# Kernel tuning notes

Hardware: AMD Instinct MI355X
Metric: run time of the kernel (lower is better)

## Reference

```python
import jax, jax.numpy as jnp
import numpy as np

N, E, G = 20000, 320000, 64
IN_DIM, HID, HEADS, NCLS = 512, 256, 2, 10
EPS = 1e-5
SLOPE = 0.2


def setup_inputs() -> dict:
    key = jax.random.key(0)
    ks = jax.random.split(key, 24)
    s = 0.02
    inp = {
        "feat": jax.random.normal(ks[0], (N, IN_DIM), jnp.float32),
        "src": jax.random.randint(ks[1], (E,), 0, N, jnp.int32),
        "dst": jax.random.randint(ks[2], (E,), 0, N, jnp.int32),
        "graph_ids": jnp.sort(jax.random.randint(ks[3], (N,), 0, G, jnp.int32)),
        # GATv2Conv params (fc_src, fc_dst, attn)
        "W_src": jax.random.normal(ks[4], (IN_DIM, HEADS * HID), jnp.float32) * s,
        "b_src": jnp.zeros((HEADS * HID,), jnp.float32),
        "W_dst": jax.random.normal(ks[5], (IN_DIM, HEADS * HID), jnp.float32) * s,
        "b_dst": jnp.zeros((HEADS * HID,), jnp.float32),
        "attn": jax.random.normal(ks[6], (HEADS, HID), jnp.float32) * s,
        # skip_lin: input_dim -> 2*hidden
        "W_skip": jax.random.normal(ks[7], (IN_DIM, 2 * HID), jnp.float32) * s,
        "b_skip": jnp.zeros((2 * HID,), jnp.float32),
        # bn1 affine
        "gamma": jnp.ones((2 * HID,), jnp.float32),
        "beta": jnp.zeros((2 * HID,), jnp.float32),
        # dim_reducer
        "W_red": jax.random.normal(ks[8], (2 * HID, HID), jnp.float32) * s,
        "b_red": jnp.zeros((HID,), jnp.float32),
        # attention-pool gate Linear(hidden, 1)
        "w_gate": jax.random.normal(ks[9], (HID, 1), jnp.float32) * s,
        "b_gate": jnp.zeros((1,), jnp.float32),
        # classifier MLP
        "W1": jax.random.normal(ks[10], (HID, HID // 2), jnp.float32) * s,
        "b1": jnp.zeros((HID // 2,), jnp.float32),
        "W2": jax.random.normal(ks[11], (HID // 2, NCLS), jnp.float32) * s,
        "b2": jnp.zeros((NCLS,), jnp.float32),
    }
    return inp


def _gatv2(feat, src, dst, W_src, b_src, W_dst, b_dst, attn):
    # feat_src/feat_dst: [N, H, D]
    fs = (feat @ W_src + b_src).reshape(N, HEADS, HID)
    fd = (feat @ W_dst + b_dst).reshape(N, HEADS, HID)
    fs_e = fs[src]                               # [E, H, D]
    m = jax.nn.leaky_relu(fs_e + fd[dst], SLOPE)  # [E, H, D]
    e = jnp.einsum("ehd,hd->eh", m, attn)         # [E, H]
    # edge softmax grouped by destination node
    e_max = jax.ops.segment_max(e, dst, num_segments=N)          # [N, H]
    e_exp = jnp.exp(e - e_max[dst])                               # [E, H]
    denom = jax.ops.segment_sum(e_exp, dst, num_segments=N)      # [N, H]
    alpha = e_exp / denom[dst]                                    # [E, H]
    out = jax.ops.segment_sum(alpha[:, :, None] * fs_e, dst, num_segments=N)
    return out  # [N, H, D]; zero rows for zero in-degree nodes


def reference(feat, src, dst, graph_ids, W_src, b_src, W_dst, b_dst, attn,
              W_skip, b_skip, gamma, beta, W_red, b_red, w_gate, b_gate,
              W1, b1, W2, b2):
    h1 = jax.nn.elu(_gatv2(feat, src, dst, W_src, b_src, W_dst, b_dst, attn))
    h1 = h1.reshape(N, HEADS * HID)
    h1 = h1 + (feat @ W_skip + b_skip)
    # BatchNorm1d (training-mode batch statistics, biased variance)
    mu = jnp.mean(h1, axis=0)
    var = jnp.mean((h1 - mu) ** 2, axis=0)
    h1 = (h1 - mu) * jax.lax.rsqrt(var + EPS) * gamma + beta
    hr = h1 @ W_red + b_red                      # [N, HID]
    # GlobalAttentionPooling: segment softmax of gate scores over each graph
    gate = hr @ w_gate + b_gate                  # [N, 1]
    g_max = jax.ops.segment_max(gate, graph_ids, num_segments=G)
    g_exp = jnp.exp(gate - g_max[graph_ids])
    g_den = jax.ops.segment_sum(g_exp, graph_ids, num_segments=G)
    a = g_exp / g_den[graph_ids]                 # [N, 1]
    h_g = jax.ops.segment_sum(a * hr, graph_ids, num_segments=G)  # [G, HID]
    # classifier (dropout = identity at inference)
    return jax.nn.relu(h_g @ W1 + b1) @ W2 + b2  # [G, NCLS]
```

## Files before the change

### kernel.cpp

```cpp
#include <hip/hip_runtime.h>
#include <math.h>

#define N_NODES 20000
#define N_EDGES 320000
#define N_GRAPH 64
#define IN_DIM  512
#define HID     256
#define F2      512
#define EPS_BN  1e-5f
#define SLOPE   0.2f
#define SCAN_BLOCKS 79
#define N_RT    157
#define RT_PAD  20096

#define SF_BLOCKS   5024
#define SW_BLOCKS   1024
#define INIT_BLOCKS 79
#define PREP_BLOCKS (SF_BLOCKS + SW_BLOCKS + INIT_BLOCKS)
#define TRIPLE_BLOCKS 1920
#define HIST_BLOCKS   1250

typedef unsigned short u16;
typedef __attribute__((ext_vector_type(8))) short bf16x8;
typedef __attribute__((ext_vector_type(4))) float floatx4;

__device__ __forceinline__ u16 bf_hi(float x) {
    unsigned int u = __float_as_uint(x);
    return (u16)((u + 0x7fffu + ((u >> 16) & 1u)) >> 16);
}
__device__ __forceinline__ float bf_val(u16 h) {
    return __uint_as_float((unsigned int)h << 16);
}
__device__ __forceinline__ void unpack2(unsigned int u, float& lo, float& hi) {
    lo = __uint_as_float(u << 16);
    hi = __uint_as_float(u & 0xffff0000u);
}
__device__ __forceinline__ float lr(float x) { return fmaxf(x, SLOPE * x); }

__device__ __forceinline__ void gload16(const u16* g, u16* l) {
    __builtin_amdgcn_global_load_lds(
        (const __attribute__((address_space(1))) void*)g,
        (__attribute__((address_space(3))) void*)l, 16, 0, 0);
}

__global__ __launch_bounds__(256) void prep_kernel(
    const float* __restrict__ feat, u16* __restrict__ Fhi,
    const float* __restrict__ Ws, const float* __restrict__ Wd,
    const float* __restrict__ Wk, const float* __restrict__ Wr,
    u16* __restrict__ Whi, u16* __restrict__ Wlo,
    int* __restrict__ counts, int* __restrict__ cursor,
    float* __restrict__ stats, float* __restrict__ h_gnum,
    float* __restrict__ gden, float* __restrict__ gate) {
    __shared__ float t[32][33];
    int b = blockIdx.x;
    int tid = threadIdx.x;
    if (b < SF_BLOCKS) {
        int i = b * 256 + tid;
        size_t base = (size_t)i * 8;
        if (i >= N_NODES * IN_DIM / 8) {
            *(uint4*)(Fhi + base) = make_uint4(0, 0, 0, 0);
            return;
        }
        float4 x0 = *(const float4*)(feat + base);
        float4 x1 = *(const float4*)(feat + base + 4);
        float xs[8] = {x0.x, x0.y, x0.z, x0.w, x1.x, x1.y, x1.z, x1.w};
        union { u16 s[8]; uint4 v; } h;
#pragma unroll
        for (int j = 0; j < 8; j++) h.s[j] = bf_hi(xs[j]);
        *(uint4*)(Fhi + base) = h.v;
    } else if (b < SF_BLOCKS + SW_BLOCKS) {
        int bb = b - SF_BLOCKS;
        int kx = bb & 15, ny = (bb >> 4) & 15, w = bb >> 8;
        int ncols = (w == 3) ? 256 : 512;
        int n0 = ny * 32;
        if (n0 >= ncols) return;
        const float* W = (w == 0) ? Ws : ((w == 1) ? Wd : ((w == 2) ? Wk : Wr));
        size_t obase = (size_t)w * 512 * 512;
        int k0 = kx * 32;
        int tx = tid & 31, ty = tid >> 5;
#pragma unroll
        for (int i = 0; i < 4; i++)
            t[ty * 4 + i][tx] = W[(size_t)(k0 + ty * 4 + i) * ncols + n0 + tx];
        __syncthreads();
#pragma unroll
        for (int i = 0; i < 4; i++) {
            float x = t[tx][ty * 4 + i];
            u16 hh = bf_hi(x);
            size_t o = obase + (size_t)(n0 + ty * 4 + i) * 512 + k0 + tx;
            Whi[o] = hh;
            Wlo[o] = bf_hi(x - bf_val(hh));
        }
    } else {
        int i = (b - SF_BLOCKS - SW_BLOCKS) * 256 + tid;
        if (i < N_NODES) { counts[i] = 0; cursor[i] = 0; gate[i] = 0.f; }
        if (i < 1024) stats[i] = 0.f;
        if (i < N_GRAPH * HID) h_gnum[i] = 0.f;
        if (i < N_GRAPH) gden[i] = 0.f;
    }
}

__global__ __launch_bounds__(256) void gemm_mfma_triple(
    const u16* __restrict__ Fhi, const u16* __restrict__ Wthi,
    const float* __restrict__ b_src, const float* __restrict__ b_dst,
    const float* __restrict__ b_skip,
    u16* __restrict__ FS16, u16* __restrict__ FD16,
    u16* __restrict__ h1hi, u16* __restrict__ h1lo,
    const int* __restrict__ dst, int* __restrict__ counts) {
    __shared__ u16 S[2][2][8192];
    int b = blockIdx.x;
    if (b >= TRIPLE_BLOCKS) {
        int e = (b - TRIPLE_BLOCKS) * 256 + threadIdx.x;
        if (e < N_EDGES) atomicAdd(&counts[dst[e]], 1);
        return;
    }
    int xcd = b & 7, slot = b >> 3;
    int rt = (slot / 12) * 8 + xcd;
    if (rt >= N_RT) return;
    int cw = slot % 12;
    int w_idx = cw >> 2;
    int col0 = (cw & 3) * 128;
    int row0 = rt * 128;
    int tid = threadIdx.x;
    int lane = tid & 63, wave = tid >> 6;
    int wm = (wave & 1) * 64, wn = (wave >> 1) * 64;
    int quad = lane >> 4, l16 = lane & 15;

    int lrow = lane >> 3;
    int kswz = ((lane & 7) ^ lrow) << 3;
    const u16* aS = Fhi + (size_t)(row0 + wave * 32 + lrow) * 512 + kswz;
    const u16* bS = Wthi + (size_t)w_idx * 512 * 512 +
                    (size_t)(col0 + wave * 32 + lrow) * 512 + kswz;

#define STAGE(buf, kk)                                                        \
    do {                                                                      \
        gload16(aS + (size_t)(kk) * 64,         &S[buf][0][(wave * 4 + 0) * 512]); \
        gload16(bS + (size_t)(kk) * 64,         &S[buf][1][(wave * 4 + 0) * 512]); \
        gload16(aS + 4096 + (size_t)(kk) * 64,  &S[buf][0][(wave * 4 + 1) * 512]); \
        gload16(bS + 4096 + (size_t)(kk) * 64,  &S[buf][1][(wave * 4 + 1) * 512]); \
        gload16(aS + 8192 + (size_t)(kk) * 64,  &S[buf][0][(wave * 4 + 2) * 512]); \
        gload16(bS + 8192 + (size_t)(kk) * 64,  &S[buf][1][(wave * 4 + 2) * 512]); \
        gload16(aS + 12288 + (size_t)(kk) * 64, &S[buf][0][(wave * 4 + 3) * 512]); \
        gload16(bS + 12288 + (size_t)(kk) * 64, &S[buf][1][(wave * 4 + 3) * 512]); \
    } while (0)

    int kx8 = (l16 & 7) << 3;
    int oS0 = (quad * 8) ^ kx8;
    int offA = (wm + l16) * 64;
    int offB = (wn + l16) * 64;

    floatx4 acc[4][4];
#pragma unroll
    for (int i = 0; i < 4; i++)
#pragma unroll
        for (int j = 0; j < 4; j++) acc[i][j] = (floatx4){0.f, 0.f, 0.f, 0.f};

    STAGE(0, 0);
    __syncthreads();

#pragma unroll
    for (int kk = 0; kk < 8; kk++) {
        if (kk < 7) STAGE((kk + 1) & 1, kk + 1);
        const u16* A = &S[kk & 1][0][0];
        const u16* B = &S[kk & 1][1][0];
        bf16x8 bv[4][2];
#pragma unroll
        for (int nt = 0; nt < 4; nt++) {
            bv[nt][0] = *(const bf16x8*)&B[offB + nt * 1024 + oS0];
            bv[nt][1] = *(const bf16x8*)&B[offB + nt * 1024 + (oS0 ^ 32)];
        }
#pragma unroll
        for (int mt = 0; mt < 4; mt++) {
            bf16x8 a0 = *(const bf16x8*)&A[offA + mt * 1024 + oS0];
            bf16x8 a1 = *(const bf16x8*)&A[offA + mt * 1024 + (oS0 ^ 32)];
#pragma unroll
            for (int nt = 0; nt < 4; nt++) {
                acc[mt][nt] = __builtin_amdgcn_mfma_f32_16x16x32_bf16(
                    bv[nt][0], a0, acc[mt][nt], 0, 0, 0);
                acc[mt][nt] = __builtin_amdgcn_mfma_f32_16x16x32_bf16(
                    bv[nt][1], a1, acc[mt][nt], 0, 0, 0);
            }
        }
        __syncthreads();
    }
#undef STAGE

    const float* bias = (w_idx == 0) ? b_src : ((w_idx == 1) ? b_dst : b_skip);
    float4 b4[4];
#pragma unroll
    for (int wt = 0; wt < 4; wt++)
        b4[wt] = *(const float4*)(bias + col0 + wn + wt * 16 + quad * 4);
#pragma unroll
    for (int ft = 0; ft < 4; ft++) {
        int m = row0 + wm + ft * 16 + l16;
        if (m >= N_NODES) continue;
        size_t rb = (size_t)m * 512;
#pragma unroll
        for (int wt = 0; wt < 4; wt++) {
            int nb = col0 + wn + wt * 16 + quad * 4;
            float v0 = acc[ft][wt][0] + b4[wt].x;
            float v1 = acc[ft][wt][1] + b4[wt].y;
            float v2 = acc[ft][wt][2] + b4[wt].z;
            float v3 = acc[ft][wt][3] + b4[wt].w;
            u16 h0 = bf_hi(v0), h1_ = bf_hi(v1), h2 = bf_hi(v2), h3 = bf_hi(v3);
            uint2 wv;
            wv.x = (unsigned)h0 | ((unsigned)h1_ << 16);
            wv.y = (unsigned)h2 | ((unsigned)h3 << 16);
            if (w_idx == 0)      *(uint2*)(FS16 + rb + nb) = wv;
            else if (w_idx == 1) *(uint2*)(FD16 + rb + nb) = wv;
            else {
                *(uint2*)(h1hi + rb + nb) = wv;
                uint2 lv;
                lv.x = (unsigned)bf_hi(v0 - bf_val(h0)) | ((unsigned)bf_hi(v1 - bf_val(h1_)) << 16);
                lv.y = (unsigned)bf_hi(v2 - bf_val(h2)) | ((unsigned)bf_hi(v3 - bf_val(h3)) << 16);
                *(uint2*)(h1lo + rb + nb) = lv;
            }
        }
    }
}

__global__ __launch_bounds__(256) void scan_local_kernel(
    const int* __restrict__ counts, int* __restrict__ row_ptr, int* __restrict__ bsum) {
    __shared__ int buf[256];
    int b = blockIdx.x, tid = threadIdx.x;
    int i = b * 256 + tid;
    buf[tid] = (i < N_NODES) ? counts[i] : 0;
    __syncthreads();
    for (int off = 1; off < 256; off <<= 1) {
        int t = (tid >= off) ? buf[tid - off] : 0;
        __syncthreads();
        buf[tid] += t;
        __syncthreads();
    }
    if (i < N_NODES) row_ptr[i + 1] = buf[tid];
    if (tid == 255) bsum[b] = buf[255];
}

__global__ __launch_bounds__(256) void scan_fixup_kernel(
    const int* __restrict__ bsum, int* __restrict__ row_ptr) {
    __shared__ int red[256];
    int b = blockIdx.x, tid = threadIdx.x;
    red[tid] = (tid < b) ? bsum[tid] : 0;
    __syncthreads();
    for (int off = 128; off > 0; off >>= 1) {
        if (tid < off) red[tid] += red[tid + off];
        __syncthreads();
    }
    int offset = red[0];
    int i = b * 256 + tid;
    if (i < N_NODES) row_ptr[i + 1] += offset;
    if (b == 0 && tid == 0) row_ptr[0] = 0;
}

__global__ void scatter_kernel(const int* __restrict__ src, const int* __restrict__ dst,
                               const int* __restrict__ row_ptr,
                               int* __restrict__ cursor, int* __restrict__ csr_src) {
    int e = blockIdx.x * blockDim.x + threadIdx.x;
    if (e < N_EDGES) {
        int d = dst[e];
        int pos = atomicAdd(&cursor[d], 1);
        csr_src[row_ptr[d] + pos] = src[e];
    }
}

__global__ __launch_bounds__(256) void edge_fused_kernel(
    const u16* __restrict__ FS16, const u16* __restrict__ FD16,
    const float* __restrict__ attn, const int* __restrict__ csr_src,
    const int* __restrict__ row_ptr,
    u16* __restrict__ h1hi, u16* __restrict__ h1lo) {
    __shared__ float red[3 * 512];
    __shared__ float den[2];
    int n = blockIdx.x, tid = threadIdx.x;
    int lane = tid & 63, wave = tid >> 6;
    int beg = row_ptr[n], end = row_ptr[n + 1], deg = end - beg;
    if (tid < 2) den[tid] = 0.f;

    float fdv[8], aw[8];
    {
        uint4 q = *(const uint4*)(FD16 + (size_t)n * 512 + 8 * lane);
        unpack2(q.x, fdv[0], fdv[1]); unpack2(q.y, fdv[2], fdv[3]);
        unpack2(q.z, fdv[4], fdv[5]); unpack2(q.w, fdv[6], fdv[7]);
        float4 a0 = *(const float4*)(attn + 8 * lane);
        float4 a1 = *(const float4*)(attn + 8 * lane + 4);
        aw[0] = a0.x; aw[1] = a0.y; aw[2] = a0.z; aw[3] = a0.w;
        aw[4] = a1.x; aw[5] = a1.y; aw[6] = a1.z; aw[7] = a1.w;
    }
    __syncthreads();

    float acc[8] = {0.f, 0.f, 0.f, 0.f, 0.f, 0.f, 0.f, 0.f};
    float dp = 0.f;
    for (int j = wave; j < deg; j += 4) {
        int s = csr_src[beg + j];
        uint4 q = *(const uint4*)(FS16 + (size_t)s * 512 + 8 * lane);
        float f[8];
        unpack2(q.x, f[0], f[1]); unpack2(q.y, f[2], f[3]);
        unpack2(q.z, f[4], f[5]); unpack2(q.w, f[6], f[7]);
        float p = 0.f;
#pragma unroll
        for (int k = 0; k < 8; k++) p += lr(f[k] + fdv[k]) * aw[k];
#pragma unroll
        for (int off = 16; off > 0; off >>= 1) p += __shfl_xor(p, off, 64);
        float ex = expf(p);
#pragma unroll
        for (int k = 0; k < 8; k++) acc[k] += ex * f[k];
        if ((lane & 31) == 0) dp += ex;
    }
    if ((lane & 31) == 0) atomicAdd(&den[lane >> 5], dp);

    if (wave > 0) {
        float* r = &red[(wave - 1) * 512 + lane * 8];
        *(float4*)(r + 0) = *(float4*)&acc[0];
        *(float4*)(r + 4) = *(float4*)&acc[4];
    }
    __syncthreads();
    if (wave == 0) {
#pragma unroll
        for (int w = 0; w < 3; w++) {
            const float* r = &red[w * 512 + lane * 8];
#pragma unroll
            for (int k = 0; k < 8; k++) acc[k] += r[k];
        }
        float d = (lane < 32) ? den[0] : den[1];
        float inv = d > 0.f ? 1.f / d : 0.f;
        size_t base = (size_t)n * 512 + 8 * lane;
        union { u16 s[8]; uint4 v; } qh, ql;
        qh.v = *(const uint4*)(h1hi + base);
        ql.v = *(const uint4*)(h1lo + base);
#pragma unroll
        for (int k = 0; k < 8; k++) {
            float skip = bf_val(qh.s[k]) + bf_val(ql.s[k]);
            float x = acc[k] * inv;
            x = x > 0.f ? x : expm1f(x);
            float y = x + skip;
            u16 hh = bf_hi(y);
            qh.s[k] = hh;
            ql.s[k] = bf_hi(y - bf_val(hh));
        }
        *(uint4*)(h1hi + base) = qh.v;
        *(uint4*)(h1lo + base) = ql.v;
    }
}

__global__ __launch_bounds__(256) void bn_stats_kernel(const u16* __restrict__ h1hi,
                                                       float* __restrict__ stats,
                                                       int rows_per_block) {
    int tid = threadIdx.x;
    int r0 = blockIdx.x * rows_per_block;
    int r1 = min(r0 + rows_per_block, N_NODES);
    float s0 = 0.f, q0 = 0.f, s1 = 0.f, q1 = 0.f;
    for (int r = r0; r < r1; r++) {
        float a = bf_val(h1hi[(size_t)r * F2 + tid]);
        float b = bf_val(h1hi[(size_t)r * F2 + 256 + tid]);
        s0 += a; q0 += a * a;
        s1 += b; q1 += b * b;
    }
    atomicAdd(&stats[tid], s0);
    atomicAdd(&stats[256 + tid], s1);
    atomicAdd(&stats[512 + tid], q0);
    atomicAdd(&stats[512 + 256 + tid], q1);
}

__global__ __launch_bounds__(256) void bn_fold_kernel(
    const float* __restrict__ stats, const float* __restrict__ gamma,
    const float* __restrict__ beta,
    const u16* __restrict__ Whi3, const u16* __restrict__ Wlo3,
    const float* __restrict__ b_red,
    u16* __restrict__ Wphi, u16* __restrict__ Wplo, float* __restrict__ bias2) {
    __shared__ float sScale[512], sShift[512];
    __shared__ float red[256];
    int n = blockIdx.x, tid = threadIdx.x;
    for (int c = tid; c < 512; c += 256) {
        float mu = stats[c] / (float)N_NODES;
        float var = stats[512 + c] / (float)N_NODES - mu * mu;
        float sc = gamma[c] * rsqrtf(var + EPS_BN);
        sScale[c] = sc;
        sShift[c] = beta[c] - mu * sc;
    }
    __syncthreads();
    float part = 0.f;
    for (int k = tid; k < 512; k += 256) {
        size_t o = (size_t)n * 512 + k;
        float w = bf_val(Whi3[o]) + bf_val(Wlo3[o]);
        part += sShift[k] * w;
        float wp = w * sScale[k];
        u16 hh = bf_hi(wp);
        Wphi[o] = hh;
        Wplo[o] = bf_hi(wp - bf_val(hh));
    }
    red[tid] = part; __syncthreads();
    for (int off = 128; off > 0; off >>= 1) {
        if (tid < off) red[tid] += red[tid + off];
        __syncthreads();
    }
    if (tid == 0) bias2[n] = b_red[n] + red[0];
}

__global__ __launch_bounds__(256) void gemm_mfma_red(
    const u16* __restrict__ Ahi, const u16* __restrict__ Alo,
    const u16* __restrict__ Bhi, const u16* __restrict__ Blo,
    const float* __restrict__ bias2, const float* __restrict__ wg,
    float* __restrict__ hr, float* __restrict__ gate) {
    __shared__ u16 AsHi[128 * 40];
    __shared__ u16 AsLo[128 * 40];
    int tid = threadIdx.x;
    int row0 = blockIdx.x * 128;
    int col0 = blockIdx.y * 128;
    int lane = tid & 63, wave = tid >> 6;
    int wm = (wave & 1) * 64, wn = (wave >> 1) * 64;
    int quad = lane >> 4, l16 = lane & 15;

    int sr = tid >> 1, sh = (tid & 1) * 16;
    int grow = row0 + sr;
    bool ok = grow < N_NODES;
    u16* sH = &AsHi[sr * 40 + sh];
    u16* sL = &AsLo[sr * 40 + sh];

    const u16* bPh[4];
    const u16* bPl[4];
#pragma unroll
    for (int nt = 0; nt < 4; nt++) {
        size_t o = (size_t)(col0 + wn + nt * 16 + l16) * 512 + quad * 8;
        bPh[nt] = Bhi + o;
        bPl[nt] = Blo + o;
    }

    floatx4 acc[4][4];
#pragma unroll
    for (int i = 0; i < 4; i++)
#pragma unroll
        for (int j = 0; j < 4; j++) acc[i][j] = (floatx4){0.f, 0.f, 0.f, 0.f};

    for (int k0 = 0; k0 < 512; k0 += 32) {
        uint4 h0 = make_uint4(0, 0, 0, 0), h1v = h0, l0 = h0, l1 = h0;
        if (ok) {
            const u16* g = Ahi + (size_t)grow * 512 + k0 + sh;
            const u16* gl = Alo + (size_t)grow * 512 + k0 + sh;
            h0 = *(const uint4*)(g);
            h1v = *(const uint4*)(g + 8);
            l0 = *(const uint4*)(gl);
            l1 = *(const uint4*)(gl + 8);
        }
        union { uint4 u; bf16x8 v; } bh[4], bl[4];
#pragma unroll
        for (int nt = 0; nt < 4; nt++) {
            bh[nt].u = *(const uint4*)(bPh[nt] + k0);
            bl[nt].u = *(const uint4*)(bPl[nt] + k0);
        }
        __syncthreads();
        *(uint4*)(sH + 0) = h0;
        *(uint4*)(sH + 8) = h1v;
        *(uint4*)(sL + 0) = l0;
        *(uint4*)(sL + 8) = l1;
        __syncthreads();
#pragma unroll
        for (int mt = 0; mt < 4; mt++) {
            int me = (wm + mt * 16 + l16) * 40 + quad * 8;
            bf16x8 ah = *(const bf16x8*)&AsHi[me];
            bf16x8 al = *(const bf16x8*)&AsLo[me];
#pragma unroll
            for (int nt = 0; nt < 4; nt++) {
                acc[mt][nt] = __builtin_amdgcn_mfma_f32_16x16x32_bf16(bh[nt].v, ah, acc[mt][nt], 0, 0, 0);
                acc[mt][nt] = __builtin_amdgcn_mfma_f32_16x16x32_bf16(bl[nt].v, ah, acc[mt][nt], 0, 0, 0);
                acc[mt][nt] = __builtin_amdgcn_mfma_f32_16x16x32_bf16(bh[nt].v, al, acc[mt][nt], 0, 0, 0);
            }
        }
    }

    float4 b4[4], w4[4];
#pragma unroll
    for (int wt = 0; wt < 4; wt++) {
        int nb = col0 + wn + wt * 16 + quad * 4;
        b4[wt] = *(const float4*)(bias2 + nb);
        w4[wt] = *(const float4*)(wg + nb);
    }
#pragma unroll
    for (int ft = 0; ft < 4; ft++) {
        int m = row0 + wm + ft * 16 + l16;
        bool ok2 = m < N_NODES;
        float g = 0.f;
#pragma unroll
        for (int wt = 0; wt < 4; wt++) {
            float4 v;
            v.x = acc[ft][wt][0] + b4[wt].x;
            v.y = acc[ft][wt][1] + b4[wt].y;
            v.z = acc[ft][wt][2] + b4[wt].z;
            v.w = acc[ft][wt][3] + b4[wt].w;
            g += v.x * w4[wt].x + v.y * w4[wt].y + v.z * w4[wt].z + v.w * w4[wt].w;
            if (ok2) *(float4*)(hr + (size_t)m * HID + col0 + wn + wt * 16 + quad * 4) = v;
        }
        g += __shfl_xor(g, 16, 64);
        g += __shfl_xor(g, 32, 64);
        if (ok2 && lane < 16) atomicAdd(&gate[m], g);
    }
}

__device__ __forceinline__ int lower_bound_dev(const int* a, int n, int v) {
    int lo = 0, hi = n;
    while (lo < hi) {
        int mid = (lo + hi) >> 1;
        if (a[mid] < v) lo = mid + 1; else hi = mid;
    }
    return lo;
}

__global__ __launch_bounds__(256) void pool_partial_kernel(
    const float* __restrict__ hr, const float* __restrict__ gate,
    const int* __restrict__ gids, float* __restrict__ h_gnum,
    float* __restrict__ gden) {
    int b = blockIdx.x;
    int g = b >> 3, part = b & 7;
    int tid = threadIdx.x;
    int start = lower_bound_dev(gids, N_NODES, g);
    int end = lower_bound_dev(gids, N_NODES, g + 1);
    int span = end - start;
    int p_beg = start + (span * part) / 8;
    int p_end = start + (span * (part + 1)) / 8;
    if (p_beg >= p_end) return;
    __shared__ float wa[256];
    __shared__ float red[256];
    float acc = 0.f, denacc = 0.f;
    for (int cbeg = p_beg; cbeg < p_end; cbeg += 256) {
        int c = min(256, p_end - cbeg);
        float e = 0.f;
        if (tid < c) { e = expf(gate[cbeg + tid]); wa[tid] = e; }
        red[tid] = (tid < c) ? e : 0.f;
        __syncthreads();
        for (int off = 128; off > 0; off >>= 1) {
            if (tid < off) red[tid] += red[tid + off];
            __syncthreads();
        }
        denacc += red[0];
        for (int i = 0; i < c; i++) acc += wa[i] * hr[(size_t)(cbeg + i) * HID + tid];
        __syncthreads();
    }
    atomicAdd(&h_gnum[g * HID + tid], acc);
    if (tid == 0) atomicAdd(&gden[g], denacc);
}

__global__ __launch_bounds__(128) void classifier_kernel(
    const float* __restrict__ h_gnum, const float* __restrict__ gden,
    const float* __restrict__ W1, const float* __restrict__ b1,
    const float* __restrict__ W2, const float* __restrict__ b2,
    float* __restrict__ out) {
    int g = blockIdx.x;
    int tid = threadIdx.x;
    __shared__ float hg[256];
    __shared__ float z1[128];
    float d = gden[g];
    float invd = d > 0.f ? 1.f / d : 0.f;
    hg[tid] = h_gnum[g * HID + tid] * invd;
    hg[tid + 128] = h_gnum[g * HID + tid + 128] * invd;
    __syncthreads();
    float a = b1[tid];
#pragma unroll 8
    for (int k = 0; k < 256; k++) a += hg[k] * W1[k * 128 + tid];
    z1[tid] = a > 0.f ? a : 0.f;
    __syncthreads();
    if (tid < 10) {
        float o = b2[tid];
#pragma unroll 8
        for (int j = 0; j < 128; j++) o += z1[j] * W2[j * 10 + tid];
        out[g * 10 + tid] = o;
    }
}

extern "C" void kernel_launch(void* const* d_in, const int* in_sizes, int n_in,
                              void* d_out, int out_size, void* d_ws, size_t ws_size,
                              hipStream_t stream) {
    const float* feat   = (const float*)d_in[0];
    const int*   src    = (const int*)d_in[1];
    const int*   dst    = (const int*)d_in[2];
    const int*   gids   = (const int*)d_in[3];
    const float* W_src  = (const float*)d_in[4];
    const float* b_src  = (const float*)d_in[5];
    const float* W_dst  = (const float*)d_in[6];
    const float* b_dst  = (const float*)d_in[7];
    const float* attn   = (const float*)d_in[8];
    const float* W_skip = (const float*)d_in[9];
    const float* b_skip = (const float*)d_in[10];
    const float* gamma  = (const float*)d_in[11];
    const float* beta   = (const float*)d_in[12];
    const float* W_red  = (const float*)d_in[13];
    const float* b_red  = (const float*)d_in[14];
    const float* w_gate = (const float*)d_in[15];
    const float* W1     = (const float*)d_in[17];
    const float* b1     = (const float*)d_in[18];
    const float* W2     = (const float*)d_in[19];
    const float* b2     = (const float*)d_in[20];
    float* out = (float*)d_out;

    char* p = (char*)d_ws;
    auto alloc = [&](size_t bytes) -> char* {
        char* r = p;
        p += (bytes + 255) & ~(size_t)255;
        return r;
    };
    u16*   FS16     = (u16*)alloc((size_t)N_NODES * F2 * 2);
    u16*   FD16     = (u16*)alloc((size_t)N_NODES * F2 * 2);
    u16*   h1hi     = (u16*)alloc((size_t)N_NODES * F2 * 2);
    u16*   h1lo     = (u16*)alloc((size_t)N_NODES * F2 * 2);
    float* gate     = (float*)alloc((size_t)N_NODES * 4);
    float* stats    = (float*)alloc(1024 * 4);
    float* bias2    = (float*)alloc(256 * 4);
    float* h_gnum   = (float*)alloc((size_t)N_GRAPH * HID * 4);
    float* gden     = (float*)alloc((size_t)N_GRAPH * 4);
    int* counts     = (int*)alloc((size_t)N_NODES * 4);
    int* row_ptr    = (int*)alloc((size_t)(N_NODES + 1) * 4);
    int* cursor     = (int*)alloc((size_t)N_NODES * 4);
    int* csr_src    = (int*)alloc((size_t)N_EDGES * 4);
    int* bsum       = (int*)alloc((size_t)SCAN_BLOCKS * 4);
    u16* Fhi        = (u16*)alloc((size_t)RT_PAD * IN_DIM * 2);
    u16* Wthi       = (u16*)alloc((size_t)4 * 512 * 512 * 2);
    u16* Wtlo       = (u16*)alloc((size_t)4 * 512 * 512 * 2);
    u16* Wphi       = (u16*)alloc((size_t)HID * 512 * 2);
    u16* Wplo       = (u16*)alloc((size_t)HID * 512 * 2);
    float* hr = (float*)Fhi;
    (void)ws_size; (void)in_sizes; (void)n_in; (void)out_size;

    const size_t WSZ = (size_t)512 * 512;

    prep_kernel<<<PREP_BLOCKS, 256, 0, stream>>>(
        feat, Fhi, W_src, W_dst, W_skip, W_red, Wthi, Wtlo,
        counts, cursor, stats, h_gnum, gden, gate);

    gemm_mfma_triple<<<TRIPLE_BLOCKS + HIST_BLOCKS, 256, 0, stream>>>(
        Fhi, Wthi, b_src, b_dst, b_skip, FS16, FD16, h1hi, h1lo, dst, counts);

    scan_local_kernel<<<SCAN_BLOCKS, 256, 0, stream>>>(counts, row_ptr, bsum);
    scan_fixup_kernel<<<SCAN_BLOCKS, 256, 0, stream>>>(bsum, row_ptr);
    scatter_kernel<<<(N_EDGES + 255) / 256, 256, 0, stream>>>(src, dst, row_ptr, cursor, csr_src);

    edge_fused_kernel<<<N_NODES, 256, 0, stream>>>(
        FS16, FD16, attn, csr_src, row_ptr, h1hi, h1lo);

    bn_stats_kernel<<<500, 256, 0, stream>>>(h1hi, stats, 40);
    bn_fold_kernel<<<HID, 256, 0, stream>>>(
        stats, gamma, beta, Wthi + 3 * WSZ, Wtlo + 3 * WSZ, b_red, Wphi, Wplo, bias2);

    dim3 g256((N_NODES + 127) / 128, 2);
    gemm_mfma_red<<<g256, 256, 0, stream>>>(
        h1hi, h1lo, Wphi, Wplo, bias2, w_gate, hr, gate);

    pool_partial_kernel<<<N_GRAPH * 8, 256, 0, stream>>>(hr, gate, gids, h_gnum, gden);

    classifier_kernel<<<N_GRAPH, 128, 0, stream>>>(h_gnum, gden, W1, b1, W2, b2, out);
}
```

Baseline: 379.8 us.

## Use fp16 packed math in edge kernel and reshuffle histogram/scan into earlier launches

Stores the projected source and destination features as fp16 instead of bf16, so the edge-attention loop can use packed half adds, max and fdot2 for the score dot product, and switches to the fast exp. The in-degree histogram moves into the prep kernel, with a memset clearing counts first, and the local scan is folded into the GEMM launch as extra blocks, which removes one kernel launch. The tradeoffs are lower precision and a narrower range (fp16 overflow) on the attention inputs, plus an extra memset call.

```diff
diff --git a/kernel.cpp b/kernel.cpp
--- a/kernel.cpp
+++ b/kernel.cpp
@@ -16,13 +16,15 @@
 #define SF_BLOCKS   5024
 #define SW_BLOCKS   1024
 #define INIT_BLOCKS 79
-#define PREP_BLOCKS (SF_BLOCKS + SW_BLOCKS + INIT_BLOCKS)
+#define HIST_BLOCKS 1250
+#define PREP_BLOCKS (SF_BLOCKS + SW_BLOCKS + INIT_BLOCKS + HIST_BLOCKS)
 #define TRIPLE_BLOCKS 1920
-#define HIST_BLOCKS   1250
 
 typedef unsigned short u16;
 typedef __attribute__((ext_vector_type(8))) short bf16x8;
 typedef __attribute__((ext_vector_type(4))) float floatx4;
+typedef _Float16 f16;
+typedef __attribute__((ext_vector_type(2))) f16 f16x2;
 
 __device__ __forceinline__ u16 bf_hi(float x) {
     unsigned int u = __float_as_uint(x);
@@ -31,11 +33,12 @@
 __device__ __forceinline__ float bf_val(u16 h) {
     return __uint_as_float((unsigned int)h << 16);
 }
-__device__ __forceinline__ void unpack2(unsigned int u, float& lo, float& hi) {
-    lo = __uint_as_float(u << 16);
-    hi = __uint_as_float(u & 0xffff0000u);
-}
-__device__ __forceinline__ float lr(float x) { return fmaxf(x, SLOPE * x); }
+__device__ __forceinline__ f16x2 h2_from_u32(unsigned int u) {
+    return __builtin_bit_cast(f16x2, u);
+}
+__device__ __forceinline__ unsigned int u32_from_h2(f16x2 h) {
+    return __builtin_bit_cast(unsigned int, h);
+}
 
 __device__ __forceinline__ void gload16(const u16* g, u16* l) {
     __builtin_amdgcn_global_load_lds(
@@ -48,7 +51,8 @@
     const float* __restrict__ Ws, const float* __restrict__ Wd,
     const float* __restrict__ Wk, const float* __restrict__ Wr,
     u16* __restrict__ Whi, u16* __restrict__ Wlo,
-    int* __restrict__ counts, int* __restrict__ cursor,
+    const int* __restrict__ dst, int* __restrict__ counts,
+    int* __restrict__ cursor,
     float* __restrict__ stats, float* __restrict__ h_gnum,
     float* __restrict__ gden, float* __restrict__ gate) {
     __shared__ float t[32][33];
@@ -90,12 +94,15 @@
             Whi[o] = hh;
             Wlo[o] = bf_hi(x - bf_val(hh));
         }
-    } else {
+    } else if (b < SF_BLOCKS + SW_BLOCKS + INIT_BLOCKS) {
         int i = (b - SF_BLOCKS - SW_BLOCKS) * 256 + tid;
-        if (i < N_NODES) { counts[i] = 0; cursor[i] = 0; gate[i] = 0.f; }
+        if (i < N_NODES) { cursor[i] = 0; gate[i] = 0.f; }
         if (i < 1024) stats[i] = 0.f;
         if (i < N_GRAPH * HID) h_gnum[i] = 0.f;
         if (i < N_GRAPH) gden[i] = 0.f;
+    } else {
+        int e = (b - SF_BLOCKS - SW_BLOCKS - INIT_BLOCKS) * 256 + tid;
+        if (e < N_EDGES) atomicAdd(&counts[dst[e]], 1);
     }
 }
 
@@ -105,12 +112,25 @@
     const float* __restrict__ b_skip,
     u16* __restrict__ FS16, u16* __restrict__ FD16,
     u16* __restrict__ h1hi, u16* __restrict__ h1lo,
-    const int* __restrict__ dst, int* __restrict__ counts) {
+    const int* __restrict__ counts, int* __restrict__ row_ptr,
+    int* __restrict__ bsum) {
     __shared__ u16 S[2][2][8192];
     int b = blockIdx.x;
+    int tid = threadIdx.x;
     if (b >= TRIPLE_BLOCKS) {
-        int e = (b - TRIPLE_BLOCKS) * 256 + threadIdx.x;
-        if (e < N_EDGES) atomicAdd(&counts[dst[e]], 1);
+        int* buf = (int*)&S[0][0][0];
+        int bb = b - TRIPLE_BLOCKS;
+        int i = bb * 256 + tid;
+        buf[tid] = (i < N_NODES) ? counts[i] : 0;
+        __syncthreads();
+        for (int off = 1; off < 256; off <<= 1) {
+            int t = (tid >= off) ? buf[tid - off] : 0;
+            __syncthreads();
+            buf[tid] += t;
+            __syncthreads();
+        }
+        if (i < N_NODES) row_ptr[i + 1] = buf[tid];
+        if (tid == 255) bsum[bb] = buf[255];
         return;
     }
     int xcd = b & 7, slot = b >> 3;
@@ -120,7 +140,6 @@
     int w_idx = cw >> 2;
     int col0 = (cw & 3) * 128;
     int row0 = rt * 128;
-    int tid = threadIdx.x;
     int lane = tid & 63, wave = tid >> 6;
     int wm = (wave & 1) * 64, wn = (wave >> 1) * 64;
     int quad = lane >> 4, l16 = lane & 15;
@@ -201,13 +220,19 @@
             float v1 = acc[ft][wt][1] + b4[wt].y;
             float v2 = acc[ft][wt][2] + b4[wt].z;
             float v3 = acc[ft][wt][3] + b4[wt].w;
-            u16 h0 = bf_hi(v0), h1_ = bf_hi(v1), h2 = bf_hi(v2), h3 = bf_hi(v3);
-            uint2 wv;
-            wv.x = (unsigned)h0 | ((unsigned)h1_ << 16);
-            wv.y = (unsigned)h2 | ((unsigned)h3 << 16);
-            if (w_idx == 0)      *(uint2*)(FS16 + rb + nb) = wv;
-            else if (w_idx == 1) *(uint2*)(FD16 + rb + nb) = wv;
-            else {
+            if (w_idx <= 1) {
+                f16x2 p0; p0[0] = (f16)v0; p0[1] = (f16)v1;
+                f16x2 p1; p1[0] = (f16)v2; p1[1] = (f16)v3;
+                uint2 wv;
+                wv.x = u32_from_h2(p0);
+                wv.y = u32_from_h2(p1);
+                if (w_idx == 0) *(uint2*)(FS16 + rb + nb) = wv;
+                else            *(uint2*)(FD16 + rb + nb) = wv;
+            } else {
+                u16 h0 = bf_hi(v0), h1_ = bf_hi(v1), h2 = bf_hi(v2), h3 = bf_hi(v3);
+                uint2 wv;
+                wv.x = (unsigned)h0 | ((unsigned)h1_ << 16);
+                wv.y = (unsigned)h2 | ((unsigned)h3 << 16);
                 *(uint2*)(h1hi + rb + nb) = wv;
                 uint2 lv;
                 lv.x = (unsigned)bf_hi(v0 - bf_val(h0)) | ((unsigned)bf_hi(v1 - bf_val(h1_)) << 16);
@@ -216,23 +241,6 @@
             }
         }
     }
-}
-
-__global__ __launch_bounds__(256) void scan_local_kernel(
-    const int* __restrict__ counts, int* __restrict__ row_ptr, int* __restrict__ bsum) {
-    __shared__ int buf[256];
-    int b = blockIdx.x, tid = threadIdx.x;
-    int i = b * 256 + tid;
-    buf[tid] = (i < N_NODES) ? counts[i] : 0;
-    __syncthreads();
-    for (int off = 1; off < 256; off <<= 1) {
-        int t = (tid >= off) ? buf[tid - off] : 0;
-        __syncthreads();
-        buf[tid] += t;
-        __syncthreads();
-    }
-    if (i < N_NODES) row_ptr[i + 1] = buf[tid];
-    if (tid == 255) bsum[b] = buf[255];
 }
 
 __global__ __launch_bounds__(256) void scan_fixup_kernel(
@@ -274,34 +282,46 @@
     int beg = row_ptr[n], end = row_ptr[n + 1], deg = end - beg;
     if (tid < 2) den[tid] = 0.f;
 
-    float fdv[8], aw[8];
+    f16x2 fd2[4], aw2[4];
     {
         uint4 q = *(const uint4*)(FD16 + (size_t)n * 512 + 8 * lane);
-        unpack2(q.x, fdv[0], fdv[1]); unpack2(q.y, fdv[2], fdv[3]);
-        unpack2(q.z, fdv[4], fdv[5]); unpack2(q.w, fdv[6], fdv[7]);
+        fd2[0] = h2_from_u32(q.x); fd2[1] = h2_from_u32(q.y);
+        fd2[2] = h2_from_u32(q.z); fd2[3] = h2_from_u32(q.w);
         float4 a0 = *(const float4*)(attn + 8 * lane);
         float4 a1 = *(const float4*)(attn + 8 * lane + 4);
-        aw[0] = a0.x; aw[1] = a0.y; aw[2] = a0.z; aw[3] = a0.w;
-        aw[4] = a1.x; aw[5] = a1.y; aw[6] = a1.z; aw[7] = a1.w;
+        aw2[0][0] = (f16)a0.x; aw2[0][1] = (f16)a0.y;
+        aw2[1][0] = (f16)a0.z; aw2[1][1] = (f16)a0.w;
+        aw2[2][0] = (f16)a1.x; aw2[2][1] = (f16)a1.y;
+        aw2[3][0] = (f16)a1.z; aw2[3][1] = (f16)a1.w;
     }
     __syncthreads();
 
+    const f16x2 sl2 = {(f16)SLOPE, (f16)SLOPE};
     float acc[8] = {0.f, 0.f, 0.f, 0.f, 0.f, 0.f, 0.f, 0.f};
     float dp = 0.f;
+    const int* cs = csr_src + beg;
+    const u16* FSb = FS16 + 8 * lane;
     for (int j = wave; j < deg; j += 4) {
-        int s = csr_src[beg + j];
-        uint4 q = *(const uint4*)(FS16 + (size_t)s * 512 + 8 * lane);
-        float f[8];
-        unpack2(q.x, f[0], f[1]); unpack2(q.y, f[2], f[3]);
-        unpack2(q.z, f[4], f[5]); unpack2(q.w, f[6], f[7]);
+        int s = cs[j];
+        uint4 q = *(const uint4*)(FSb + (size_t)s * 512);
+        f16x2 f2[4];
+        f2[0] = h2_from_u32(q.x); f2[1] = h2_from_u32(q.y);
+        f2[2] = h2_from_u32(q.z); f2[3] = h2_from_u32(q.w);
         float p = 0.f;
 #pragma unroll
-        for (int k = 0; k < 8; k++) p += lr(f[k] + fdv[k]) * aw[k];
+        for (int k = 0; k < 4; k++) {
+            f16x2 sm = f2[k] + fd2[k];
+            f16x2 m = __builtin_elementwise_max(sm, sm * sl2);
+            p = __builtin_amdgcn_fdot2(m, aw2[k], p, false);
+        }
 #pragma unroll
         for (int off = 16; off > 0; off >>= 1) p += __shfl_xor(p, off, 64);
-        float ex = expf(p);
-#pragma unroll
-        for (int k = 0; k < 8; k++) acc[k] += ex * f[k];
+        float ex = __expf(p);
+#pragma unroll
+        for (int k = 0; k < 4; k++) {
+            acc[2 * k]     += ex * (float)f2[k][0];
+            acc[2 * k + 1] += ex * (float)f2[k][1];
+        }
         if ((lane & 31) == 0) dp += ex;
     }
     if ((lane & 31) == 0) atomicAdd(&den[lane >> 5], dp);
@@ -618,14 +638,16 @@
 
     const size_t WSZ = (size_t)512 * 512;
 
+    hipMemsetAsync(counts, 0, (size_t)N_NODES * 4, stream);
+
     prep_kernel<<<PREP_BLOCKS, 256, 0, stream>>>(
         feat, Fhi, W_src, W_dst, W_skip, W_red, Wthi, Wtlo,
-        counts, cursor, stats, h_gnum, gden, gate);
-
-    gemm_mfma_triple<<<TRIPLE_BLOCKS + HIST_BLOCKS, 256, 0, stream>>>(
-        Fhi, Wthi, b_src, b_dst, b_skip, FS16, FD16, h1hi, h1lo, dst, counts);
-
-    scan_local_kernel<<<SCAN_BLOCKS, 256, 0, stream>>>(counts, row_ptr, bsum);
+        dst, counts, cursor, stats, h_gnum, gden, gate);
+
+    gemm_mfma_triple<<<TRIPLE_BLOCKS + SCAN_BLOCKS, 256, 0, stream>>>(
+        Fhi, Wthi, b_src, b_dst, b_skip, FS16, FD16, h1hi, h1lo,
+        counts, row_ptr, bsum);
+
     scan_fixup_kernel<<<SCAN_BLOCKS, 256, 0, stream>>>(bsum, row_ptr);
     scatter_kernel<<<(N_EDGES + 255) / 256, 256, 0, stream>>>(src, dst, row_ptr, cursor, csr_src);
 
```

Result: no change. 373.1 us (-1.8%).
